# Performance work log

Measured on AMD Instinct MI355X. Metric: run time of the kernel, lower is better.

The kernel has to match this reference:

```python
import jax, jax.numpy as jnp
import numpy as np
from jax import lax

B, N, SEG, T = 64, 19, 15, 400
FIN, HID, K, NH, DM, FF, L, NC = 64, 128, 4, 4, 64, 128, 4, 3
EPS = 1e-5


def setup_inputs() -> dict:
    key = jax.random.key(0)
    ks = jax.random.split(key, 40)
    nrm = lambda i, s, sc=0.05: jax.random.normal(ks[i], s, dtype=jnp.float32) * sc
    inp = {
        "X": jax.random.normal(ks[0], (B, N, SEG, T), dtype=jnp.float32),
        "A_hat": jax.random.uniform(ks[1], (B, K, SEG, N, N), dtype=jnp.float32),
        "conv1_w": nrm(2, (32, 1, 25)), "conv1_b": nrm(3, (32,)),
        "conv2_w": nrm(4, (64, 32, 9)), "conv2_b": nrm(5, (64,)),
        "g1_W": nrm(6, (HID, FIN)), "g1_q": nrm(7, (K,), 1.0),
        "g1_bn_g": jnp.ones((HID,)), "g1_bn_b": jnp.zeros((HID,)),
        "g1_bn_m": jnp.zeros((HID,)), "g1_bn_v": jnp.ones((HID,)),
        "g2_W": nrm(8, (FIN, HID)), "g2_q": nrm(9, (K,), 1.0),
        "g2_bn_g": jnp.ones((FIN,)), "g2_bn_b": jnp.zeros((FIN,)),
        "g2_bn_m": jnp.zeros((FIN,)), "g2_bn_v": jnp.ones((FIN,)),
        "cls_token": nrm(10, (1, 1, DM), 0.02), "pos_emb": nrm(11, (1, SEG + 1, DM), 0.02),
        "t_wqkv": nrm(12, (L, 3 * DM, DM)), "t_bqkv": nrm(13, (L, 3 * DM)),
        "t_wo": nrm(14, (L, DM, DM)), "t_bo": nrm(15, (L, DM)),
        "t_ln1g": jnp.ones((L, DM)), "t_ln1b": jnp.zeros((L, DM)),
        "t_w1": nrm(16, (L, FF, DM)), "t_b1": nrm(17, (L, FF)),
        "t_w2": nrm(18, (L, DM, FF)), "t_b2": nrm(19, (L, DM)),
        "t_ln2g": jnp.ones((L, DM)), "t_ln2b": jnp.zeros((L, DM)),
        "clf_w": nrm(20, (NC, DM)), "clf_b": nrm(21, (NC,)),
    }
    return inp


def _ln(x, g, b):
    mu = x.mean(-1, keepdims=True)
    v = ((x - mu) ** 2).mean(-1, keepdims=True)
    return (x - mu) * lax.rsqrt(v + EPS) * g + b


def _maxpool(x, w):  # x: [M, C, T]
    return lax.reduce_window(x, -jnp.inf, lax.max, (1, 1, w), (1, 1, w), "VALID")


def _temporal_encoder(X, c1w, c1b, c2w, c2b):
    # X: [B, SEG, N, T] -> [B, SEG, N, FIN]
    x = X.reshape(-1, 1, T)
    dn = ("NCH", "OIH", "NCH")
    x = lax.conv_general_dilated(x, c1w, (4,), [(12, 12)], dimension_numbers=dn) + c1b[None, :, None]
    x = _maxpool(jax.nn.relu(x), 4)                      # [M,32,25]
    x = lax.conv_general_dilated(x, c2w, (2,), [(4, 4)], dimension_numbers=dn) + c2b[None, :, None]
    x = _maxpool(jax.nn.relu(x), 2)                      # [M,64,6]
    x = x.mean(-1)                                       # AdaptiveAvgPool1d(1)
    return x.reshape(B, SEG, N, FIN)


def _gcn(Xf, A, W, q, g, b, m, v):
    alpha = jax.nn.softmax(q)                            # [K]
    AX = jnp.einsum("bksnm,bsmf->bksnf", A, Xf)          # K-hop diffusion
    Hk = jnp.einsum("bksnf,of->bksno", AX, W)            # shared linear
    H = jnp.einsum("k,bksno->bsno", alpha, Hk)           # attn-weighted hop mix
    H = (H - m) * lax.rsqrt(v + EPS) * g + b             # eval-mode BatchNorm1d
    return jax.nn.relu(H)


def _forward(X, A_hat, conv1_w, conv1_b, conv2_w, conv2_b,
             g1_W, g1_q, g1_bn_g, g1_bn_b, g1_bn_m, g1_bn_v,
             g2_W, g2_q, g2_bn_g, g2_bn_b, g2_bn_m, g2_bn_v,
             cls_token, pos_emb, t_wqkv, t_bqkv, t_wo, t_bo,
             t_ln1g, t_ln1b, t_w1, t_b1, t_w2, t_b2, t_ln2g, t_ln2b,
             clf_w, clf_b):
    Xs = X.reshape(-1, N, SEG, T).transpose(0, 2, 1, 3)  # [B,SEG,N,T]
    feat = _temporal_encoder(Xs, conv1_w, conv1_b, conv2_w, conv2_b)
    H = _gcn(feat, A_hat, g1_W, g1_q, g1_bn_g, g1_bn_b, g1_bn_m, g1_bn_v)
    H = _gcn(H, A_hat, g2_W, g2_q, g2_bn_g, g2_bn_b, g2_bn_m, g2_bn_v)
    g = H.mean(axis=2)                                   # node-mean -> [B,SEG,DM]
    x = jnp.concatenate([jnp.broadcast_to(cls_token, (B, 1, DM)), g], axis=1)
    x = x + pos_emb[:, : SEG + 1]
    dh = DM // NH
    for l in range(L):
        qkv = x @ t_wqkv[l].T + t_bqkv[l]
        qh, kh, vh = [u.reshape(B, SEG + 1, NH, dh).transpose(0, 2, 1, 3)
                      for u in jnp.split(qkv, 3, axis=-1)]
        attn = jax.nn.softmax(jnp.einsum("bhqd,bhkd->bhqk", qh, kh) / jnp.sqrt(jnp.float32(dh)), axis=-1)
        o = jnp.einsum("bhqk,bhkd->bhqd", attn, vh).transpose(0, 2, 1, 3).reshape(B, SEG + 1, DM)
        x = _ln(x + o @ t_wo[l].T + t_bo[l], t_ln1g[l], t_ln1b[l])
        ff = jax.nn.relu(x @ t_w1[l].T + t_b1[l]) @ t_w2[l].T + t_b2[l]
        x = _ln(x + ff, t_ln2g[l], t_ln2b[l])
    return x[:, 0] @ clf_w.T + clf_b                     # [B, NC]


def reference(X, A_hat, conv1_w, conv1_b, conv2_w, conv2_b,
              g1_W, g1_q, g1_bn_g, g1_bn_b, g1_bn_m, g1_bn_v,
              g2_W, g2_q, g2_bn_g, g2_bn_b, g2_bn_m, g2_bn_v,
              cls_token, pos_emb, t_wqkv, t_bqkv, t_wo, t_bo,
              t_ln1g, t_ln1b, t_w1, t_b1, t_w2, t_b2, t_ln2g, t_ln2b,
              clf_w, clf_b):
    return _forward(X, A_hat, conv1_w, conv1_b, conv2_w, conv2_b,
                    g1_W, g1_q, g1_bn_g, g1_bn_b, g1_bn_m, g1_bn_v,
                    g2_W, g2_q, g2_bn_g, g2_bn_b, g2_bn_m, g2_bn_v,
                    cls_token, pos_emb, t_wqkv, t_bqkv, t_wo, t_bo,
                    t_ln1g, t_ln1b, t_w1, t_b1, t_w2, t_b2, t_ln2g, t_ln2b,
                    clf_w, clf_b)
```

## Files before the change

### kernel.cpp

```cpp
#include <hip/hip_runtime.h>
#include <cmath>

#define B_ 64
#define N_ 19
#define SEG_ 15
#define T_ 400
#define FIN_ 64
#define HID_ 128
#define K_ 4
#define NH_ 4
#define DM_ 64
#define FF_ 128
#define L_ 4
#define NC_ 3
#define EPS_ 1e-5f

typedef __attribute__((ext_vector_type(8))) short bf16x8;
typedef __attribute__((ext_vector_type(4))) short bf16x4;
typedef __attribute__((ext_vector_type(4))) float f32x4;
typedef unsigned short ushort_t;

__device__ __forceinline__ ushort_t f2bf(float x) {
  union { float f; unsigned u; } a; a.f = x;
  unsigned r = a.u + 0x7fffu + ((a.u >> 16) & 1u);
  return (ushort_t)(r >> 16);
}
__device__ __forceinline__ float bf2f(ushort_t h) {
  union { unsigned u; float f; } a; a.u = ((unsigned)h) << 16;
  return a.f;
}

__global__ __launch_bounds__(256) void k_prep(
    const float* __restrict__ c1w, const float* __restrict__ c2w,
    const float* __restrict__ wqkv, const float* __restrict__ wo,
    const float* __restrict__ w1, const float* __restrict__ w2,
    const float* __restrict__ g1W, const float* __restrict__ g2W,
    ushort_t* __restrict__ bt,
    ushort_t* __restrict__ Th, ushort_t* __restrict__ Tl,
    ushort_t* __restrict__ W1h, ushort_t* __restrict__ W1l,
    ushort_t* __restrict__ W2h, ushort_t* __restrict__ W2l,
    ushort_t* __restrict__ C1h, ushort_t* __restrict__ C1l) {
  int gid = blockIdx.x * 256 + threadIdx.x;
  if (gid < 18944) {
    int oc = gid / 296, k = gid - oc * 296;
    int ic = k & 31, kk = k >> 5;
    ushort_t v = 0;
    if (kk < 9) v = f2bf(c2w[oc * 288 + ic * 9 + kk]);
    bt[gid] = v;
  } else if (gid < 68096) {
    int i = gid - 18944;
    int l = i / 12288, r = i % 12288;
    float v = wqkv[i];
    ushort_t h = f2bf(v);
    int dst = l * 32768 + r;
    Th[dst] = h; Tl[dst] = f2bf(v - bf2f(h));
  } else if (gid < 84480) {
    int i = gid - 68096;
    int l = i / 4096, r = i % 4096;
    float v = wo[i];
    ushort_t h = f2bf(v);
    int dst = l * 32768 + 12288 + r;
    Th[dst] = h; Tl[dst] = f2bf(v - bf2f(h));
  } else if (gid < 117248) {
    int i = gid - 84480;
    int l = i / 8192, r = i % 8192;
    float v = w1[i];
    ushort_t h = f2bf(v);
    int dst = l * 32768 + 16384 + r;
    Th[dst] = h; Tl[dst] = f2bf(v - bf2f(h));
  } else if (gid < 150016) {
    int i = gid - 117248;
    int l = i / 8192, r = i % 8192;
    float v = w2[i];
    ushort_t h = f2bf(v);
    int dst = l * 32768 + 24576 + r;
    Th[dst] = h; Tl[dst] = f2bf(v - bf2f(h));
  } else if (gid < 158208) {
    int i = gid - 150016;
    float v = g1W[i];
    ushort_t h = f2bf(v);
    W1h[i] = h;
    W1l[i] = f2bf(v - bf2f(h));
  } else if (gid < 166400) {
    int i = gid - 158208;
    float v = g2W[i];
    ushort_t h = f2bf(v);
    W2h[i] = h;
    W2l[i] = f2bf(v - bf2f(h));
  } else if (gid < 167424) {
    int i = gid - 166400;
    int oc = i >> 5, kk = i & 31;
    float v = (kk < 25) ? c1w[oc * 25 + kk] : 0.f;
    ushort_t h = f2bf(v);
    C1h[i] = h;
    C1l[i] = f2bf(v - bf2f(h));
  }
}

#define RPB 4
#define ICP 40
#define P1R 40
#define OFF_XPH 0
#define OFF_XPL 3840
#define OFF_P1  7680
#define SMEM_T  20480

__global__ __launch_bounds__(256, 4) void k_temporal(
    const float* __restrict__ X, const float* __restrict__ c1b,
    const float* __restrict__ c2b,
    const ushort_t* __restrict__ C1h, const ushort_t* __restrict__ C1l,
    const ushort_t* __restrict__ BmatT, float* __restrict__ Xf) {
  __shared__ __align__(16) unsigned char smem[SMEM_T];
  ushort_t* xph = (ushort_t*)(smem + OFF_XPH);
  ushort_t* xpl = (ushort_t*)(smem + OFF_XPL);
  ushort_t* p1T = (ushort_t*)(smem + OFF_P1);
  float* Dbuf = (float*)smem;

  const int tid = threadIdx.x;
  const int row0 = blockIdx.x * RPB;
  const int lane = tid & 63, wv = tid >> 6;
  const int quad = lane >> 4, nl = lane & 15;

  for (int i = tid; i < 3200; i += 256) ((unsigned*)p1T)[i] = 0u;
  for (int r = 0; r < RPB; ++r) {
    const int gr = row0 + r;
    const int n = gr % N_;
    const int s = (gr / N_) % SEG_;
    const int b = gr / (N_ * SEG_);
    const float* xin = X + (((size_t)b * N_ + n) * SEG_ + s) * T_ - 12;
    for (int i = tid; i < 480; i += 256) {
      float v = (i >= 12 && i < 412) ? xin[i] : 0.f;
      ushort_t h = f2bf(v);
      xph[r * 480 + i] = h;
      xpl[r * 480 + i] = f2bf(v - bf2f(h));
    }
  }
  __syncthreads();

  {
    bf16x8 bh0 = *(const bf16x8*)(C1h + nl * 32 + quad * 8);
    bf16x8 bh1 = *(const bf16x8*)(C1h + (16 + nl) * 32 + quad * 8);
    bf16x8 bl0 = *(const bf16x8*)(C1l + nl * 32 + quad * 8);
    bf16x8 bl1 = *(const bf16x8*)(C1l + (16 + nl) * 32 + quad * 8);
    const float bias0 = c1b[nl], bias1 = c1b[16 + nl];
    for (int t = wv; t < 28; t += 4) {
      const int r = t / 7, mt = t - r * 7;
      const int aoff = r * 480 + mt * 64 + nl * 4 + quad * 8;
      union { bf16x4 q[2]; bf16x8 v; } ah, al;
      ah.q[0] = *(const bf16x4*)(xph + aoff);
      ah.q[1] = *(const bf16x4*)(xph + aoff + 4);
      al.q[0] = *(const bf16x4*)(xpl + aoff);
      al.q[1] = *(const bf16x4*)(xpl + aoff + 4);
      f32x4 a0 = (f32x4){0.f, 0.f, 0.f, 0.f};
      a0 = __builtin_amdgcn_mfma_f32_16x16x32_bf16(ah.v, bh0, a0, 0, 0, 0);
      a0 = __builtin_amdgcn_mfma_f32_16x16x32_bf16(al.v, bh0, a0, 0, 0, 0);
      a0 = __builtin_amdgcn_mfma_f32_16x16x32_bf16(ah.v, bl0, a0, 0, 0, 0);
      f32x4 a1 = (f32x4){0.f, 0.f, 0.f, 0.f};
      a1 = __builtin_amdgcn_mfma_f32_16x16x32_bf16(ah.v, bh1, a1, 0, 0, 0);
      a1 = __builtin_amdgcn_mfma_f32_16x16x32_bf16(al.v, bh1, a1, 0, 0, 0);
      a1 = __builtin_amdgcn_mfma_f32_16x16x32_bf16(ah.v, bl1, a1, 0, 0, 0);
      const int j = mt * 4 + quad;
      if (j < 25) {
        float m0 = fmaxf(fmaxf(a0[0], a0[1]), fmaxf(a0[2], a0[3]));
        float m1 = fmaxf(fmaxf(a1[0], a1[1]), fmaxf(a1[2], a1[3]));
        p1T[(r * P1R + j + 4) * ICP + nl] = f2bf(fmaxf(m0 + bias0, 0.f));
        p1T[(r * P1R + j + 4) * ICP + 16 + nl] = f2bf(fmaxf(m1 + bias1, 0.f));
      }
    }
  }
  __syncthreads();

  f32x4 acc[4];
  int abase[4];
#pragma unroll
  for (int tm = 0; tm < 4; ++tm) {
    acc[tm] = (f32x4){0.f, 0.f, 0.f, 0.f};
    int m = tm * 16 + nl;
    int rl = m / 14;
    int op = m - rl * 14;
    if (rl > 3) rl = 3;
    if (op > 13) op = 13;
    abase[tm] = (rl * P1R + 2 * op) * ICP + quad * 8;
  }
  const ushort_t* brow = BmatT + (wv * 16 + nl) * 296 + quad * 8;
#pragma unroll
  for (int kk = 0; kk < 9; ++kk) {
    bf16x8 bfr = *(const bf16x8*)(brow + kk * 32);
#pragma unroll
    for (int tm = 0; tm < 4; ++tm) {
      bf16x8 afr = *(const bf16x8*)(p1T + abase[tm] + kk * ICP);
      acc[tm] = __builtin_amdgcn_mfma_f32_16x16x32_bf16(afr, bfr, acc[tm], 0, 0, 0);
    }
  }
  __syncthreads();

#pragma unroll
  for (int tm = 0; tm < 4; ++tm)
#pragma unroll
    for (int rg = 0; rg < 4; ++rg)
      Dbuf[(tm * 16 + quad * 4 + rg) * 66 + wv * 16 + nl] = acc[tm][rg];
  __syncthreads();

  for (int o = tid; o < RPB * 64; o += 256) {
    int rl = o >> 6, oc = o & 63;
    float bias = c2b[oc];
    const float* dr = Dbuf + (rl * 14) * 66 + oc;
    float s = 0.f;
#pragma unroll
    for (int jj = 0; jj < 6; ++jj) {
      float v = fmaxf(dr[(2 * jj) * 66], dr[(2 * jj + 1) * 66]) + bias;
      s += fmaxf(v, 0.f);
    }
    Xf[(size_t)(row0 + rl) * FIN_ + oc] = s * (1.f / 6.f);
  }
}

__global__ __launch_bounds__(256, 2) void k_gcn(
    const float* __restrict__ A, const float* __restrict__ Xf,
    const ushort_t* __restrict__ W1h, const ushort_t* __restrict__ W1l,
    const ushort_t* __restrict__ W2h, const ushort_t* __restrict__ W2l,
    const float* __restrict__ q1, const float* __restrict__ q2,
    const float* __restrict__ b1g, const float* __restrict__ b1b,
    const float* __restrict__ b1m, const float* __restrict__ b1v,
    const float* __restrict__ b2g, const float* __restrict__ b2b,
    const float* __restrict__ b2m, const float* __restrict__ b2v,
    float* __restrict__ G) {
  const int bs = blockIdx.x;
  const int b = bs / SEG_;
  const int s = bs % SEG_;
  const int tid = threadIdx.x;
  const int lane = tid & 63, wv = tid >> 6;
  const int quad = lane >> 4, nl = lane & 15;

  __shared__ __align__(16) ushort_t xh[32 * 72], xl[32 * 72];
  __shared__ __align__(16) ushort_t Hh[32 * 136], Hl[32 * 136];
  __shared__ __align__(16) ushort_t a1h[32 * 40], a1l[32 * 40];
  __shared__ __align__(16) ushort_t a2h[32 * 40], a2l[32 * 40];
  __shared__ __align__(16) ushort_t yTh[128 * 40], yTl[128 * 40];
  __shared__ float zbuf[N_ * 64];
  __shared__ float sc1[HID_], sh1[HID_], sc2[FIN_], sh2[FIN_];

  for (int i = tid; i < 32 * 72 / 2; i += 256) {
    ((unsigned*)xh)[i] = 0u; ((unsigned*)xl)[i] = 0u;
  }
  for (int i = tid; i < 32 * 136 / 2; i += 256) {
    ((unsigned*)Hh)[i] = 0u; ((unsigned*)Hl)[i] = 0u;
  }
  for (int i = tid; i < 32 * 40 / 2; i += 256) {
    ((unsigned*)a1h)[i] = 0u; ((unsigned*)a1l)[i] = 0u;
    ((unsigned*)a2h)[i] = 0u; ((unsigned*)a2l)[i] = 0u;
  }
  for (int o = tid; o < HID_; o += 256) {
    float sc = b1g[o] * rsqrtf(b1v[o] + EPS_);
    sc1[o] = sc; sh1[o] = b1b[o] - b1m[o] * sc;
  }
  for (int o = tid; o < FIN_; o += 256) {
    float sc = b2g[o] * rsqrtf(b2v[o] + EPS_);
    sc2[o] = sc; sh2[o] = b2b[o] - b2m[o] * sc;
  }
  __syncthreads();

  {
    float p0 = q1[0], p1 = q1[1], p2 = q1[2], p3 = q1[3];
    float mx = fmaxf(fmaxf(p0, p1), fmaxf(p2, p3));
    float e0 = expf(p0 - mx), e1 = expf(p1 - mx), e2 = expf(p2 - mx), e3 = expf(p3 - mx);
    float inv = 1.f / (e0 + e1 + e2 + e3);
    float a0 = e0 * inv, a1 = e1 * inv, a2 = e2 * inv, a3 = e3 * inv;
    float r0 = q2[0], r1 = q2[1], r2 = q2[2], r3 = q2[3];
    float mx2 = fmaxf(fmaxf(r0, r1), fmaxf(r2, r3));
    float f0 = expf(r0 - mx2), f1 = expf(r1 - mx2), f2 = expf(r2 - mx2), f3 = expf(r3 - mx2);
    float inv2 = 1.f / (f0 + f1 + f2 + f3);
    float c0 = f0 * inv2, c1 = f1 * inv2, c2 = f2 * inv2, c3 = f3 * inv2;
    const size_t kstride = (size_t)SEG_ * N_ * N_;
    const float* Ab = A + ((size_t)b * K_ * SEG_ + s) * (N_ * N_);
    for (int i = tid; i < N_ * N_; i += 256) {
      int n = i / N_, m = i - n * N_;
      float v0 = Ab[i], v1 = Ab[i + kstride], v2 = Ab[i + 2 * kstride], v3 = Ab[i + 3 * kstride];
      float w1v = a0 * v0 + a1 * v1 + a2 * v2 + a3 * v3;
      float w2v = c0 * v0 + c1 * v1 + c2 * v2 + c3 * v3;
      ushort_t h1 = f2bf(w1v);
      a1h[n * 40 + m] = h1; a1l[n * 40 + m] = f2bf(w1v - bf2f(h1));
      ushort_t h2 = f2bf(w2v);
      a2h[n * 40 + m] = h2; a2l[n * 40 + m] = f2bf(w2v - bf2f(h2));
    }
  }
  {
    const float* xb = Xf + (size_t)bs * N_ * FIN_;
    for (int i = tid; i < N_ * FIN_; i += 256) {
      int r = i >> 6, f = i & 63;
      float v = xb[i];
      ushort_t h = f2bf(v);
      xh[r * 72 + f] = h;
      xl[r * 72 + f] = f2bf(v - bf2f(h));
    }
  }
  __syncthreads();

#pragma unroll
  for (int mtl = 0; mtl < 2; ++mtl) {
    const int om = (wv * 2 + mtl) * 16;
#pragma unroll
    for (int nt = 0; nt < 2; ++nt) {
      f32x4 acc = (f32x4){0.f, 0.f, 0.f, 0.f};
#pragma unroll
      for (int ks = 0; ks < 2; ++ks) {
        bf16x8 ah = *(const bf16x8*)(W1h + (om + nl) * 64 + ks * 32 + quad * 8);
        bf16x8 al = *(const bf16x8*)(W1l + (om + nl) * 64 + ks * 32 + quad * 8);
        bf16x8 bh = *(const bf16x8*)(xh + (nt * 16 + nl) * 72 + ks * 32 + quad * 8);
        bf16x8 bl = *(const bf16x8*)(xl + (nt * 16 + nl) * 72 + ks * 32 + quad * 8);
        acc = __builtin_amdgcn_mfma_f32_16x16x32_bf16(ah, bh, acc, 0, 0, 0);
        acc = __builtin_amdgcn_mfma_f32_16x16x32_bf16(al, bh, acc, 0, 0, 0);
        acc = __builtin_amdgcn_mfma_f32_16x16x32_bf16(ah, bl, acc, 0, 0, 0);
      }
#pragma unroll
      for (int r = 0; r < 4; ++r) {
        int o = om + quad * 4 + r, node = nt * 16 + nl;
        float v = acc[r];
        ushort_t hh = f2bf(v);
        yTh[o * 40 + node] = hh;
        yTl[o * 40 + node] = f2bf(v - bf2f(hh));
      }
    }
  }
  __syncthreads();

#pragma unroll
  for (int mt = 0; mt < 2; ++mt) {
#pragma unroll
    for (int ntl = 0; ntl < 2; ++ntl) {
      const int nt = wv * 2 + ntl;
      f32x4 acc = (f32x4){0.f, 0.f, 0.f, 0.f};
      bf16x8 ah = *(const bf16x8*)(a1h + (mt * 16 + nl) * 40 + quad * 8);
      bf16x8 al = *(const bf16x8*)(a1l + (mt * 16 + nl) * 40 + quad * 8);
      bf16x8 bh = *(const bf16x8*)(yTh + (nt * 16 + nl) * 40 + quad * 8);
      bf16x8 bl = *(const bf16x8*)(yTl + (nt * 16 + nl) * 40 + quad * 8);
      acc = __builtin_amdgcn_mfma_f32_16x16x32_bf16(ah, bh, acc, 0, 0, 0);
      acc = __builtin_amdgcn_mfma_f32_16x16x32_bf16(al, bh, acc, 0, 0, 0);
      acc = __builtin_amdgcn_mfma_f32_16x16x32_bf16(ah, bl, acc, 0, 0, 0);
      const int o = nt * 16 + nl;
      const float sc = sc1[o], sh = sh1[o];
#pragma unroll
      for (int r = 0; r < 4; ++r) {
        int node = mt * 16 + quad * 4 + r;
        if (node < N_) {
          float h = fmaxf(acc[r] * sc + sh, 0.f);
          ushort_t hh = f2bf(h);
          Hh[node * 136 + o] = hh;
          Hl[node * 136 + o] = f2bf(h - bf2f(hh));
        }
      }
    }
  }
  __syncthreads();

  {
    const int om = wv * 16;
#pragma unroll
    for (int nt = 0; nt < 2; ++nt) {
      f32x4 acc = (f32x4){0.f, 0.f, 0.f, 0.f};
#pragma unroll
      for (int ks = 0; ks < 4; ++ks) {
        bf16x8 ah = *(const bf16x8*)(W2h + (om + nl) * 128 + ks * 32 + quad * 8);
        bf16x8 al = *(const bf16x8*)(W2l + (om + nl) * 128 + ks * 32 + quad * 8);
        bf16x8 bh = *(const bf16x8*)(Hh + (nt * 16 + nl) * 136 + ks * 32 + quad * 8);
        bf16x8 bl = *(const bf16x8*)(Hl + (nt * 16 + nl) * 136 + ks * 32 + quad * 8);
        acc = __builtin_amdgcn_mfma_f32_16x16x32_bf16(ah, bh, acc, 0, 0, 0);
        acc = __builtin_amdgcn_mfma_f32_16x16x32_bf16(al, bh, acc, 0, 0, 0);
        acc = __builtin_amdgcn_mfma_f32_16x16x32_bf16(ah, bl, acc, 0, 0, 0);
      }
#pragma unroll
      for (int r = 0; r < 4; ++r) {
        int o2 = om + quad * 4 + r, node = nt * 16 + nl;
        float v = acc[r];
        ushort_t hh = f2bf(v);
        yTh[o2 * 40 + node] = hh;
        yTl[o2 * 40 + node] = f2bf(v - bf2f(hh));
      }
    }
  }
  __syncthreads();

#pragma unroll
  for (int mt = 0; mt < 2; ++mt) {
    f32x4 acc = (f32x4){0.f, 0.f, 0.f, 0.f};
    bf16x8 ah = *(const bf16x8*)(a2h + (mt * 16 + nl) * 40 + quad * 8);
    bf16x8 al = *(const bf16x8*)(a2l + (mt * 16 + nl) * 40 + quad * 8);
    bf16x8 bh = *(const bf16x8*)(yTh + (wv * 16 + nl) * 40 + quad * 8);
    bf16x8 bl = *(const bf16x8*)(yTl + (wv * 16 + nl) * 40 + quad * 8);
    acc = __builtin_amdgcn_mfma_f32_16x16x32_bf16(ah, bh, acc, 0, 0, 0);
    acc = __builtin_amdgcn_mfma_f32_16x16x32_bf16(al, bh, acc, 0, 0, 0);
    acc = __builtin_amdgcn_mfma_f32_16x16x32_bf16(ah, bl, acc, 0, 0, 0);
    const int o2 = wv * 16 + nl;
    const float sc = sc2[o2], sh = sh2[o2];
#pragma unroll
    for (int r = 0; r < 4; ++r) {
      int node = mt * 16 + quad * 4 + r;
      if (node < N_)
        zbuf[node * 64 + o2] = fmaxf(acc[r] * sc + sh, 0.f);
    }
  }
  __syncthreads();

  if (tid < FIN_) {
    float ssum = 0.f;
#pragma unroll
    for (int nn = 0; nn < N_; ++nn) ssum += zbuf[nn * 64 + tid];
    G[(size_t)bs * FIN_ + tid] = ssum * (1.f / (float)N_);
  }
}

__global__ __launch_bounds__(64, 1) void k_transformer(
    const float* __restrict__ G, const float* __restrict__ cls,
    const float* __restrict__ pos,
    const ushort_t* __restrict__ Th, const ushort_t* __restrict__ Tl,
    const float* __restrict__ bqkv, const float* __restrict__ bo,
    const float* __restrict__ ln1g, const float* __restrict__ ln1b,
    const float* __restrict__ b1, const float* __restrict__ b2,
    const float* __restrict__ ln2g, const float* __restrict__ ln2b,
    const float* __restrict__ clfw, const float* __restrict__ clfb,
    float* __restrict__ out) {
  const int b = blockIdx.x;
  const int lane = threadIdx.x;
  const int quad = lane >> 4, nl = lane & 15;

  __shared__ float xbuf[16 * 64];
  __shared__ __align__(16) ushort_t xh[16 * 72], xl[16 * 72];
  __shared__ float qkvb[16 * 196];
  __shared__ float scb[16 * 17];
  __shared__ __align__(16) ushort_t oh[16 * 72], ol[16 * 72];
  __shared__ __align__(16) ushort_t h1h[16 * 136], h1l[16 * 136];
  __shared__ float tmpb[16 * 64];

#pragma unroll
  for (int g = 0; g < 4; ++g) {
    const int t = g * 4 + quad;
    float4 base = (t == 0) ? ((const float4*)cls)[nl]
                           : ((const float4*)(G + ((size_t)b * SEG_ + (t - 1)) * DM_))[nl];
    float4 p = ((const float4*)(pos + t * DM_))[nl];
    float4 v;
    v.x = base.x + p.x; v.y = base.y + p.y;
    v.z = base.z + p.z; v.w = base.w + p.w;
    ((float4*)(xbuf + t * 64))[nl] = v;
    const int bi = t * 72 + nl * 4;
    ushort_t h0 = f2bf(v.x), h1 = f2bf(v.y), h2 = f2bf(v.z), h3 = f2bf(v.w);
    xh[bi + 0] = h0; xh[bi + 1] = h1; xh[bi + 2] = h2; xh[bi + 3] = h3;
    xl[bi + 0] = f2bf(v.x - bf2f(h0));
    xl[bi + 1] = f2bf(v.y - bf2f(h1));
    xl[bi + 2] = f2bf(v.z - bf2f(h2));
    xl[bi + 3] = f2bf(v.w - bf2f(h3));
  }

  for (int l = 0; l < L_; ++l) {
    const ushort_t* TH = Th + l * 32768;
    const ushort_t* TL = Tl + l * 32768;

#pragma unroll
    for (int nt = 0; nt < 12; ++nt) {
      f32x4 acc = (f32x4){0.f, 0.f, 0.f, 0.f};
#pragma unroll
      for (int ks = 0; ks < 2; ++ks) {
        bf16x8 ah = *(const bf16x8*)(xh + nl * 72 + ks * 32 + quad * 8);
        bf16x8 al = *(const bf16x8*)(xl + nl * 72 + ks * 32 + quad * 8);
        bf16x8 bh = *(const bf16x8*)(TH + (nt * 16 + nl) * 64 + ks * 32 + quad * 8);
        bf16x8 bl = *(const bf16x8*)(TL + (nt * 16 + nl) * 64 + ks * 32 + quad * 8);
        acc = __builtin_amdgcn_mfma_f32_16x16x32_bf16(ah, bh, acc, 0, 0, 0);
        acc = __builtin_amdgcn_mfma_f32_16x16x32_bf16(al, bh, acc, 0, 0, 0);
        acc = __builtin_amdgcn_mfma_f32_16x16x32_bf16(ah, bl, acc, 0, 0, 0);
      }
      const int j = nt * 16 + nl;
      const float bias = bqkv[l * 192 + j];
#pragma unroll
      for (int r = 0; r < 4; ++r)
        qkvb[(quad * 4 + r) * 196 + j] = acc[r] + bias;
    }

#pragma unroll
    for (int h = 0; h < NH_; ++h) {
      float sc[4];
      const float4* qr = (const float4*)(qkvb + nl * 196 + h * 16);
      float4 q0 = qr[0], q1 = qr[1], q2 = qr[2], q3 = qr[3];
#pragma unroll
      for (int uu = 0; uu < 4; ++uu) {
        const float4* kr = (const float4*)(qkvb + (quad * 4 + uu) * 196 + 64 + h * 16);
        float4 k0 = kr[0], k1 = kr[1], k2 = kr[2], k3 = kr[3];
        float a = q0.x * k0.x + q0.y * k0.y + q0.z * k0.z + q0.w * k0.w
                + q1.x * k1.x + q1.y * k1.y + q1.z * k1.z + q1.w * k1.w
                + q2.x * k2.x + q2.y * k2.y + q2.z * k2.z + q2.w * k2.w
                + q3.x * k3.x + q3.y * k3.y + q3.z * k3.z + q3.w * k3.w;
        sc[uu] = a * 0.25f;
      }
      float mx = fmaxf(fmaxf(sc[0], sc[1]), fmaxf(sc[2], sc[3]));
      mx = fmaxf(mx, __shfl_xor(mx, 16));
      mx = fmaxf(mx, __shfl_xor(mx, 32));
      float e[4];
      float sum = 0.f;
#pragma unroll
      for (int uu = 0; uu < 4; ++uu) { e[uu] = expf(sc[uu] - mx); sum += e[uu]; }
      sum += __shfl_xor(sum, 16);
      sum += __shfl_xor(sum, 32);
      const float is = 1.f / sum;
      float* prow = &scb[nl * 17];
#pragma unroll
      for (int uu = 0; uu < 4; ++uu) prow[quad * 4 + uu] = e[uu] * is;
      float o0 = 0.f, o1 = 0.f, o2 = 0.f, o3 = 0.f;
#pragma unroll
      for (int u = 0; u < 16; ++u) {
        float p = prow[u];
        float4 vv = *(const float4*)(qkvb + u * 196 + 128 + h * 16 + quad * 4);
        o0 += p * vv.x; o1 += p * vv.y; o2 += p * vv.z; o3 += p * vv.w;
      }
      const int eb = nl * 72 + h * 16 + quad * 4;
      ushort_t h0 = f2bf(o0), h1 = f2bf(o1), h2 = f2bf(o2), h3 = f2bf(o3);
      oh[eb + 0] = h0; oh[eb + 1] = h1; oh[eb + 2] = h2; oh[eb + 3] = h3;
      ol[eb + 0] = f2bf(o0 - bf2f(h0));
      ol[eb + 1] = f2bf(o1 - bf2f(h1));
      ol[eb + 2] = f2bf(o2 - bf2f(h2));
      ol[eb + 3] = f2bf(o3 - bf2f(h3));
    }

#pragma unroll
    for (int nt = 0; nt < 4; ++nt) {
      f32x4 acc = (f32x4){0.f, 0.f, 0.f, 0.f};
#pragma unroll
      for (int ks = 0; ks < 2; ++ks) {
        bf16x8 ah = *(const bf16x8*)(oh + nl * 72 + ks * 32 + quad * 8);
        bf16x8 al = *(const bf16x8*)(ol + nl * 72 + ks * 32 + quad * 8);
        bf16x8 bh = *(const bf16x8*)(TH + 12288 + (nt * 16 + nl) * 64 + ks * 32 + quad * 8);
        bf16x8 bl = *(const bf16x8*)(TL + 12288 + (nt * 16 + nl) * 64 + ks * 32 + quad * 8);
        acc = __builtin_amdgcn_mfma_f32_16x16x32_bf16(ah, bh, acc, 0, 0, 0);
        acc = __builtin_amdgcn_mfma_f32_16x16x32_bf16(al, bh, acc, 0, 0, 0);
        acc = __builtin_amdgcn_mfma_f32_16x16x32_bf16(ah, bl, acc, 0, 0, 0);
      }
      const int d = nt * 16 + nl;
      const float bias = bo[l * 64 + d];
#pragma unroll
      for (int r = 0; r < 4; ++r) {
        int t = quad * 4 + r;
        tmpb[t * 64 + d] = xbuf[t * 64 + d] + acc[r] + bias;
      }
    }

#pragma unroll
    for (int g = 0; g < 4; ++g) {
      const int t = g * 4 + quad;
      float4 v = ((const float4*)(tmpb + t * 64))[nl];
      float s = v.x + v.y + v.z + v.w;
      s += __shfl_xor(s, 1); s += __shfl_xor(s, 2);
      s += __shfl_xor(s, 4); s += __shfl_xor(s, 8);
      float mu = s * (1.f / 64.f);
      float d0 = v.x - mu, d1 = v.y - mu, d2 = v.z - mu, d3 = v.w - mu;
      float vr = d0 * d0 + d1 * d1 + d2 * d2 + d3 * d3;
      vr += __shfl_xor(vr, 1); vr += __shfl_xor(vr, 2);
      vr += __shfl_xor(vr, 4); vr += __shfl_xor(vr, 8);
      float rs = rsqrtf(vr * (1.f / 64.f) + EPS_);
      float4 g4 = ((const float4*)(ln1g + l * 64))[nl];
      float4 b4 = ((const float4*)(ln1b + l * 64))[nl];
      float4 o4;
      o4.x = d0 * rs * g4.x + b4.x; o4.y = d1 * rs * g4.y + b4.y;
      o4.z = d2 * rs * g4.z + b4.z; o4.w = d3 * rs * g4.w + b4.w;
      ((float4*)(xbuf + t * 64))[nl] = o4;
      const int bi = t * 72 + nl * 4;
      ushort_t h0 = f2bf(o4.x), h1 = f2bf(o4.y), h2 = f2bf(o4.z), h3 = f2bf(o4.w);
      xh[bi + 0] = h0; xh[bi + 1] = h1; xh[bi + 2] = h2; xh[bi + 3] = h3;
      xl[bi + 0] = f2bf(o4.x - bf2f(h0));
      xl[bi + 1] = f2bf(o4.y - bf2f(h1));
      xl[bi + 2] = f2bf(o4.z - bf2f(h2));
      xl[bi + 3] = f2bf(o4.w - bf2f(h3));
    }

#pragma unroll
    for (int nt = 0; nt < 8; ++nt) {
      f32x4 acc = (f32x4){0.f, 0.f, 0.f, 0.f};
#pragma unroll
      for (int ks = 0; ks < 2; ++ks) {
        bf16x8 ah = *(const bf16x8*)(xh + nl * 72 + ks * 32 + quad * 8);
        bf16x8 al = *(const bf16x8*)(xl + nl * 72 + ks * 32 + quad * 8);
        bf16x8 bh = *(const bf16x8*)(TH + 16384 + (nt * 16 + nl) * 64 + ks * 32 + quad * 8);
        bf16x8 bl = *(const bf16x8*)(TL + 16384 + (nt * 16 + nl) * 64 + ks * 32 + quad * 8);
        acc = __builtin_amdgcn_mfma_f32_16x16x32_bf16(ah, bh, acc, 0, 0, 0);
        acc = __builtin_amdgcn_mfma_f32_16x16x32_bf16(al, bh, acc, 0, 0, 0);
        acc = __builtin_amdgcn_mfma_f32_16x16x32_bf16(ah, bl, acc, 0, 0, 0);
      }
      const int f = nt * 16 + nl;
      const float bias = b1[l * 128 + f];
#pragma unroll
      for (int r = 0; r < 4; ++r) {
        int t = quad * 4 + r;
        float v = fmaxf(acc[r] + bias, 0.f);
        ushort_t hh = f2bf(v);
        h1h[t * 136 + f] = hh;
        h1l[t * 136 + f] = f2bf(v - bf2f(hh));
      }
    }

#pragma unroll
    for (int nt = 0; nt < 4; ++nt) {
      f32x4 acc = (f32x4){0.f, 0.f, 0.f, 0.f};
#pragma unroll
      for (int ks = 0; ks < 4; ++ks) {
        bf16x8 ah = *(const bf16x8*)(h1h + nl * 136 + ks * 32 + quad * 8);
        bf16x8 al = *(const bf16x8*)(h1l + nl * 136 + ks * 32 + quad * 8);
        bf16x8 bh = *(const bf16x8*)(TH + 24576 + (nt * 16 + nl) * 128 + ks * 32 + quad * 8);
        bf16x8 bl = *(const bf16x8*)(TL + 24576 + (nt * 16 + nl) * 128 + ks * 32 + quad * 8);
        acc = __builtin_amdgcn_mfma_f32_16x16x32_bf16(ah, bh, acc, 0, 0, 0);
        acc = __builtin_amdgcn_mfma_f32_16x16x32_bf16(al, bh, acc, 0, 0, 0);
        acc = __builtin_amdgcn_mfma_f32_16x16x32_bf16(ah, bl, acc, 0, 0, 0);
      }
      const int d = nt * 16 + nl;
      const float bias = b2[l * 64 + d];
#pragma unroll
      for (int r = 0; r < 4; ++r) {
        int t = quad * 4 + r;
        tmpb[t * 64 + d] = xbuf[t * 64 + d] + acc[r] + bias;
      }
    }

#pragma unroll
    for (int g = 0; g < 4; ++g) {
      const int t = g * 4 + quad;
      float4 v = ((const float4*)(tmpb + t * 64))[nl];
      float s = v.x + v.y + v.z + v.w;
      s += __shfl_xor(s, 1); s += __shfl_xor(s, 2);
      s += __shfl_xor(s, 4); s += __shfl_xor(s, 8);
      float mu = s * (1.f / 64.f);
      float d0 = v.x - mu, d1 = v.y - mu, d2 = v.z - mu, d3 = v.w - mu;
      float vr = d0 * d0 + d1 * d1 + d2 * d2 + d3 * d3;
      vr += __shfl_xor(vr, 1); vr += __shfl_xor(vr, 2);
      vr += __shfl_xor(vr, 4); vr += __shfl_xor(vr, 8);
      float rs = rsqrtf(vr * (1.f / 64.f) + EPS_);
      float4 g4 = ((const float4*)(ln2g + l * 64))[nl];
      float4 b4 = ((const float4*)(ln2b + l * 64))[nl];
      float4 o4;
      o4.x = d0 * rs * g4.x + b4.x; o4.y = d1 * rs * g4.y + b4.y;
      o4.z = d2 * rs * g4.z + b4.z; o4.w = d3 * rs * g4.w + b4.w;
      ((float4*)(xbuf + t * 64))[nl] = o4;
      const int bi = t * 72 + nl * 4;
      ushort_t h0 = f2bf(o4.x), h1 = f2bf(o4.y), h2 = f2bf(o4.z), h3 = f2bf(o4.w);
      xh[bi + 0] = h0; xh[bi + 1] = h1; xh[bi + 2] = h2; xh[bi + 3] = h3;
      xl[bi + 0] = f2bf(o4.x - bf2f(h0));
      xl[bi + 1] = f2bf(o4.y - bf2f(h1));
      xl[bi + 2] = f2bf(o4.z - bf2f(h2));
      xl[bi + 3] = f2bf(o4.w - bf2f(h3));
    }
  }

  if (lane < NC_) {
    float acc = clfb[lane];
    const float* wr = &clfw[lane * DM_];
    for (int d = 0; d < DM_; ++d) acc += xbuf[d] * wr[d];
    out[b * NC_ + lane] = acc;
  }
}

extern "C" void kernel_launch(void* const* d_in, const int* in_sizes, int n_in,
                              void* d_out, int out_size, void* d_ws, size_t ws_size,
                              hipStream_t stream) {
  (void)in_sizes; (void)n_in; (void)out_size; (void)ws_size;
  const float* X    = (const float*)d_in[0];
  const float* A    = (const float*)d_in[1];
  const float* c1w  = (const float*)d_in[2];
  const float* c1b  = (const float*)d_in[3];
  const float* c2w  = (const float*)d_in[4];
  const float* c2b  = (const float*)d_in[5];
  const float* g1W  = (const float*)d_in[6];
  const float* g1q  = (const float*)d_in[7];
  const float* g1g  = (const float*)d_in[8];
  const float* g1b  = (const float*)d_in[9];
  const float* g1m  = (const float*)d_in[10];
  const float* g1v  = (const float*)d_in[11];
  const float* g2W  = (const float*)d_in[12];
  const float* g2q  = (const float*)d_in[13];
  const float* g2g  = (const float*)d_in[14];
  const float* g2b  = (const float*)d_in[15];
  const float* g2m  = (const float*)d_in[16];
  const float* g2v  = (const float*)d_in[17];
  const float* cls  = (const float*)d_in[18];
  const float* pos  = (const float*)d_in[19];
  const float* wqkv = (const float*)d_in[20];
  const float* bqkv = (const float*)d_in[21];
  const float* wo   = (const float*)d_in[22];
  const float* bo   = (const float*)d_in[23];
  const float* ln1g = (const float*)d_in[24];
  const float* ln1b = (const float*)d_in[25];
  const float* w1   = (const float*)d_in[26];
  const float* b1   = (const float*)d_in[27];
  const float* w2   = (const float*)d_in[28];
  const float* b2   = (const float*)d_in[29];
  const float* ln2g = (const float*)d_in[30];
  const float* ln2b = (const float*)d_in[31];
  const float* clfw = (const float*)d_in[32];
  const float* clfb = (const float*)d_in[33];
  float* out = (float*)d_out;

  char* wsb = (char*)d_ws;
  ushort_t* BmatT = (ushort_t*)(wsb + 0);
  ushort_t* Th  = (ushort_t*)(wsb + 37888);
  ushort_t* Tl  = (ushort_t*)(wsb + 300032);
  ushort_t* W1h = (ushort_t*)(wsb + 562176);
  ushort_t* W1l = (ushort_t*)(wsb + 578560);
  ushort_t* W2h = (ushort_t*)(wsb + 594944);
  ushort_t* W2l = (ushort_t*)(wsb + 611328);
  ushort_t* C1h = (ushort_t*)(wsb + 627712);
  ushort_t* C1l = (ushort_t*)(wsb + 629760);
  float* Xf   = (float*)(wsb + 631808);
  float* G    = (float*)(wsb + 5301248);

  k_prep<<<654, 256, 0, stream>>>(c1w, c2w, wqkv, wo, w1, w2, g1W, g2W,
                                  BmatT, Th, Tl, W1h, W1l, W2h, W2l, C1h, C1l);
  k_temporal<<<B_ * SEG_ * N_ / RPB, 256, 0, stream>>>(
      X, c1b, c2b, C1h, C1l, BmatT, Xf);
  k_gcn<<<B_ * SEG_, 256, 0, stream>>>(A, Xf, W1h, W1l, W2h, W2l,
                                       g1q, g2q, g1g, g1b, g1m, g1v,
                                       g2g, g2b, g2m, g2v, G);
  k_transformer<<<B_, 64, 0, stream>>>(G, cls, pos, Th, Tl,
                                       bqkv, bo, ln1g, ln1b, b1, b2, ln2g, ln2b,
                                       clfw, clfb, out);
}
```

Baseline: 245.6 us.

## Prefetch transformer weight fragments into registers and interleave MFMA chains

In the transformer layer loop, the weight fragments for QKV, output projection and both FFN matmuls are now loaded from global memory ahead of use. QKV weights are double-buffered across pairs of output tiles, and the other weights are loaded early so the loads overlap the attention and layernorm work. The activation fragments are hoisted out of the tile loops, and two independent accumulators are interleaved so consecutive MFMAs do not depend on each other. Biases and layernorm parameters are also loaded early. The cost is much higher register pressure, which could cause spills or lower occupancy.

```diff
diff --git a/kernel.cpp b/kernel.cpp
--- a/kernel.cpp
+++ b/kernel.cpp
@@ -29,6 +29,7 @@
   union { unsigned u; float f; } a; a.u = ((unsigned)h) << 16;
   return a.f;
 }
+#define MFMA(a, b, c) __builtin_amdgcn_mfma_f32_16x16x32_bf16((a), (b), (c), 0, 0, 0)
 
 __global__ __launch_bounds__(256) void k_prep(
     const float* __restrict__ c1w, const float* __restrict__ c2w,
@@ -152,13 +153,13 @@
       al.q[0] = *(const bf16x4*)(xpl + aoff);
       al.q[1] = *(const bf16x4*)(xpl + aoff + 4);
       f32x4 a0 = (f32x4){0.f, 0.f, 0.f, 0.f};
-      a0 = __builtin_amdgcn_mfma_f32_16x16x32_bf16(ah.v, bh0, a0, 0, 0, 0);
-      a0 = __builtin_amdgcn_mfma_f32_16x16x32_bf16(al.v, bh0, a0, 0, 0, 0);
-      a0 = __builtin_amdgcn_mfma_f32_16x16x32_bf16(ah.v, bl0, a0, 0, 0, 0);
+      a0 = MFMA(ah.v, bh0, a0);
+      a0 = MFMA(al.v, bh0, a0);
+      a0 = MFMA(ah.v, bl0, a0);
       f32x4 a1 = (f32x4){0.f, 0.f, 0.f, 0.f};
-      a1 = __builtin_amdgcn_mfma_f32_16x16x32_bf16(ah.v, bh1, a1, 0, 0, 0);
-      a1 = __builtin_amdgcn_mfma_f32_16x16x32_bf16(al.v, bh1, a1, 0, 0, 0);
-      a1 = __builtin_amdgcn_mfma_f32_16x16x32_bf16(ah.v, bl1, a1, 0, 0, 0);
+      a1 = MFMA(ah.v, bh1, a1);
+      a1 = MFMA(al.v, bh1, a1);
+      a1 = MFMA(ah.v, bl1, a1);
       const int j = mt * 4 + quad;
       if (j < 25) {
         float m0 = fmaxf(fmaxf(a0[0], a0[1]), fmaxf(a0[2], a0[3]));
@@ -189,7 +190,7 @@
 #pragma unroll
     for (int tm = 0; tm < 4; ++tm) {
       bf16x8 afr = *(const bf16x8*)(p1T + abase[tm] + kk * ICP);
-      acc[tm] = __builtin_amdgcn_mfma_f32_16x16x32_bf16(afr, bfr, acc[tm], 0, 0, 0);
+      acc[tm] = MFMA(afr, bfr, acc[tm]);
     }
   }
   __syncthreads();
@@ -308,9 +309,9 @@
         bf16x8 al = *(const bf16x8*)(W1l + (om + nl) * 64 + ks * 32 + quad * 8);
         bf16x8 bh = *(const bf16x8*)(xh + (nt * 16 + nl) * 72 + ks * 32 + quad * 8);
         bf16x8 bl = *(const bf16x8*)(xl + (nt * 16 + nl) * 72 + ks * 32 + quad * 8);
-        acc = __builtin_amdgcn_mfma_f32_16x16x32_bf16(ah, bh, acc, 0, 0, 0);
-        acc = __builtin_amdgcn_mfma_f32_16x16x32_bf16(al, bh, acc, 0, 0, 0);
-        acc = __builtin_amdgcn_mfma_f32_16x16x32_bf16(ah, bl, acc, 0, 0, 0);
+        acc = MFMA(ah, bh, acc);
+        acc = MFMA(al, bh, acc);
+        acc = MFMA(ah, bl, acc);
       }
 #pragma unroll
       for (int r = 0; r < 4; ++r) {
@@ -334,9 +335,9 @@
       bf16x8 al = *(const bf16x8*)(a1l + (mt * 16 + nl) * 40 + quad * 8);
       bf16x8 bh = *(const bf16x8*)(yTh + (nt * 16 + nl) * 40 + quad * 8);
       bf16x8 bl = *(const bf16x8*)(yTl + (nt * 16 + nl) * 40 + quad * 8);
-      acc = __builtin_amdgcn_mfma_f32_16x16x32_bf16(ah, bh, acc, 0, 0, 0);
-      acc = __builtin_amdgcn_mfma_f32_16x16x32_bf16(al, bh, acc, 0, 0, 0);
-      acc = __builtin_amdgcn_mfma_f32_16x16x32_bf16(ah, bl, acc, 0, 0, 0);
+      acc = MFMA(ah, bh, acc);
+      acc = MFMA(al, bh, acc);
+      acc = MFMA(ah, bl, acc);
       const int o = nt * 16 + nl;
       const float sc = sc1[o], sh = sh1[o];
 #pragma unroll
@@ -364,9 +365,9 @@
         bf16x8 al = *(const bf16x8*)(W2l + (om + nl) * 128 + ks * 32 + quad * 8);
         bf16x8 bh = *(const bf16x8*)(Hh + (nt * 16 + nl) * 136 + ks * 32 + quad * 8);
         bf16x8 bl = *(const bf16x8*)(Hl + (nt * 16 + nl) * 136 + ks * 32 + quad * 8);
-        acc = __builtin_amdgcn_mfma_f32_16x16x32_bf16(ah, bh, acc, 0, 0, 0);
-        acc = __builtin_amdgcn_mfma_f32_16x16x32_bf16(al, bh, acc, 0, 0, 0);
-        acc = __builtin_amdgcn_mfma_f32_16x16x32_bf16(ah, bl, acc, 0, 0, 0);
+        acc = MFMA(ah, bh, acc);
+        acc = MFMA(al, bh, acc);
+        acc = MFMA(ah, bl, acc);
       }
 #pragma unroll
       for (int r = 0; r < 4; ++r) {
@@ -387,9 +388,9 @@
     bf16x8 al = *(const bf16x8*)(a2l + (mt * 16 + nl) * 40 + quad * 8);
     bf16x8 bh = *(const bf16x8*)(yTh + (wv * 16 + nl) * 40 + quad * 8);
     bf16x8 bl = *(const bf16x8*)(yTl + (wv * 16 + nl) * 40 + quad * 8);
-    acc = __builtin_amdgcn_mfma_f32_16x16x32_bf16(ah, bh, acc, 0, 0, 0);
-    acc = __builtin_amdgcn_mfma_f32_16x16x32_bf16(al, bh, acc, 0, 0, 0);
-    acc = __builtin_amdgcn_mfma_f32_16x16x32_bf16(ah, bl, acc, 0, 0, 0);
+    acc = MFMA(ah, bh, acc);
+    acc = MFMA(al, bh, acc);
+    acc = MFMA(ah, bl, acc);
     const int o2 = wv * 16 + nl;
     const float sc = sc2[o2], sh = sh2[o2];
 #pragma unroll
@@ -454,25 +455,87 @@
     const ushort_t* TH = Th + l * 32768;
     const ushort_t* TL = Tl + l * 32768;
 
-#pragma unroll
-    for (int nt = 0; nt < 12; ++nt) {
-      f32x4 acc = (f32x4){0.f, 0.f, 0.f, 0.f};
+    {
+      float qb[12];
+#pragma unroll
+      for (int nt = 0; nt < 12; ++nt) qb[nt] = bqkv[l * 192 + nt * 16 + nl];
+      bf16x8 xah[2], xal[2];
 #pragma unroll
       for (int ks = 0; ks < 2; ++ks) {
-        bf16x8 ah = *(const bf16x8*)(xh + nl * 72 + ks * 32 + quad * 8);
-        bf16x8 al = *(const bf16x8*)(xl + nl * 72 + ks * 32 + quad * 8);
-        bf16x8 bh = *(const bf16x8*)(TH + (nt * 16 + nl) * 64 + ks * 32 + quad * 8);
-        bf16x8 bl = *(const bf16x8*)(TL + (nt * 16 + nl) * 64 + ks * 32 + quad * 8);
-        acc = __builtin_amdgcn_mfma_f32_16x16x32_bf16(ah, bh, acc, 0, 0, 0);
-        acc = __builtin_amdgcn_mfma_f32_16x16x32_bf16(al, bh, acc, 0, 0, 0);
-        acc = __builtin_amdgcn_mfma_f32_16x16x32_bf16(ah, bl, acc, 0, 0, 0);
-      }
-      const int j = nt * 16 + nl;
-      const float bias = bqkv[l * 192 + j];
-#pragma unroll
-      for (int r = 0; r < 4; ++r)
-        qkvb[(quad * 4 + r) * 196 + j] = acc[r] + bias;
-    }
+        xah[ks] = *(const bf16x8*)(xh + nl * 72 + ks * 32 + quad * 8);
+        xal[ks] = *(const bf16x8*)(xl + nl * 72 + ks * 32 + quad * 8);
+      }
+      bf16x8 wh[2][2][2], wl[2][2][2];
+#pragma unroll
+      for (int tp = 0; tp < 2; ++tp)
+#pragma unroll
+        for (int ks = 0; ks < 2; ++ks) {
+          wh[0][tp][ks] = *(const bf16x8*)(TH + (tp * 16 + nl) * 64 + ks * 32 + quad * 8);
+          wl[0][tp][ks] = *(const bf16x8*)(TL + (tp * 16 + nl) * 64 + ks * 32 + quad * 8);
+        }
+#pragma unroll
+      for (int pr = 0; pr < 6; ++pr) {
+        const int cb = pr & 1, nb = cb ^ 1;
+        if (pr < 5) {
+#pragma unroll
+          for (int tp = 0; tp < 2; ++tp)
+#pragma unroll
+            for (int ks = 0; ks < 2; ++ks) {
+              const int nt = (pr + 1) * 2 + tp;
+              wh[nb][tp][ks] = *(const bf16x8*)(TH + (nt * 16 + nl) * 64 + ks * 32 + quad * 8);
+              wl[nb][tp][ks] = *(const bf16x8*)(TL + (nt * 16 + nl) * 64 + ks * 32 + quad * 8);
+            }
+        }
+        f32x4 a0 = (f32x4){0.f, 0.f, 0.f, 0.f};
+        f32x4 a1 = (f32x4){0.f, 0.f, 0.f, 0.f};
+#pragma unroll
+        for (int ks = 0; ks < 2; ++ks) {
+          a0 = MFMA(xah[ks], wh[cb][0][ks], a0);
+          a1 = MFMA(xah[ks], wh[cb][1][ks], a1);
+          a0 = MFMA(xal[ks], wh[cb][0][ks], a0);
+          a1 = MFMA(xal[ks], wh[cb][1][ks], a1);
+          a0 = MFMA(xah[ks], wl[cb][0][ks], a0);
+          a1 = MFMA(xah[ks], wl[cb][1][ks], a1);
+        }
+        const int j0 = (pr * 2) * 16 + nl, j1 = (pr * 2 + 1) * 16 + nl;
+#pragma unroll
+        for (int r = 0; r < 4; ++r) {
+          qkvb[(quad * 4 + r) * 196 + j0] = a0[r] + qb[pr * 2];
+          qkvb[(quad * 4 + r) * 196 + j1] = a1[r] + qb[pr * 2 + 1];
+        }
+      }
+    }
+
+    bf16x8 pwh[2][2][2], pwl[2][2][2];
+#pragma unroll
+    for (int pp = 0; pp < 2; ++pp)
+#pragma unroll
+      for (int tp = 0; tp < 2; ++tp)
+#pragma unroll
+        for (int ks = 0; ks < 2; ++ks) {
+          const int nt = pp * 2 + tp;
+          pwh[pp][tp][ks] = *(const bf16x8*)(TH + 12288 + (nt * 16 + nl) * 64 + ks * 32 + quad * 8);
+          pwl[pp][tp][ks] = *(const bf16x8*)(TL + 12288 + (nt * 16 + nl) * 64 + ks * 32 + quad * 8);
+        }
+    float pb[4];
+#pragma unroll
+    for (int nt = 0; nt < 4; ++nt) pb[nt] = bo[l * 64 + nt * 16 + nl];
+    float4 g1v4 = ((const float4*)(ln1g + l * 64))[nl];
+    float4 b1v4 = ((const float4*)(ln1b + l * 64))[nl];
+    bf16x8 fwh[4][2][2], fwl[4][2][2];
+#pragma unroll
+    for (int pp = 0; pp < 4; ++pp)
+#pragma unroll
+      for (int tp = 0; tp < 2; ++tp)
+#pragma unroll
+        for (int ks = 0; ks < 2; ++ks) {
+          const int nt = pp * 2 + tp;
+          fwh[pp][tp][ks] = *(const bf16x8*)(TH + 16384 + (nt * 16 + nl) * 64 + ks * 32 + quad * 8);
+          fwl[pp][tp][ks] = *(const bf16x8*)(TL + 16384 + (nt * 16 + nl) * 64 + ks * 32 + quad * 8);
+        }
+    float fb[8];
+#pragma unroll
+    for (int nt = 0; nt < 8; ++nt) fb[nt] = b1[l * 128 + nt * 16 + nl];
 
 #pragma unroll
     for (int h = 0; h < NH_; ++h) {
@@ -518,27 +581,52 @@
       ol[eb + 3] = f2bf(o3 - bf2f(h3));
     }
 
-#pragma unroll
-    for (int nt = 0; nt < 4; ++nt) {
-      f32x4 acc = (f32x4){0.f, 0.f, 0.f, 0.f};
+    {
+      bf16x8 oah[2], oal[2];
 #pragma unroll
       for (int ks = 0; ks < 2; ++ks) {
-        bf16x8 ah = *(const bf16x8*)(oh + nl * 72 + ks * 32 + quad * 8);
-        bf16x8 al = *(const bf16x8*)(ol + nl * 72 + ks * 32 + quad * 8);
-        bf16x8 bh = *(const bf16x8*)(TH + 12288 + (nt * 16 + nl) * 64 + ks * 32 + quad * 8);
-        bf16x8 bl = *(const bf16x8*)(TL + 12288 + (nt * 16 + nl) * 64 + ks * 32 + quad * 8);
-        acc = __builtin_amdgcn_mfma_f32_16x16x32_bf16(ah, bh, acc, 0, 0, 0);
-        acc = __builtin_amdgcn_mfma_f32_16x16x32_bf16(al, bh, acc, 0, 0, 0);
-        acc = __builtin_amdgcn_mfma_f32_16x16x32_bf16(ah, bl, acc, 0, 0, 0);
-      }
-      const int d = nt * 16 + nl;
-      const float bias = bo[l * 64 + d];
-#pragma unroll
-      for (int r = 0; r < 4; ++r) {
-        int t = quad * 4 + r;
-        tmpb[t * 64 + d] = xbuf[t * 64 + d] + acc[r] + bias;
-      }
-    }
+        oah[ks] = *(const bf16x8*)(oh + nl * 72 + ks * 32 + quad * 8);
+        oal[ks] = *(const bf16x8*)(ol + nl * 72 + ks * 32 + quad * 8);
+      }
+#pragma unroll
+      for (int pp = 0; pp < 2; ++pp) {
+        f32x4 a0 = (f32x4){0.f, 0.f, 0.f, 0.f};
+        f32x4 a1 = (f32x4){0.f, 0.f, 0.f, 0.f};
+#pragma unroll
+        for (int ks = 0; ks < 2; ++ks) {
+          a0 = MFMA(oah[ks], pwh[pp][0][ks], a0);
+          a1 = MFMA(oah[ks], pwh[pp][1][ks], a1);
+          a0 = MFMA(oal[ks], pwh[pp][0][ks], a0);
+          a1 = MFMA(oal[ks], pwh[pp][1][ks], a1);
+          a0 = MFMA(oah[ks], pwl[pp][0][ks], a0);
+          a1 = MFMA(oah[ks], pwl[pp][1][ks], a1);
+        }
+        const int d0 = (pp * 2) * 16 + nl, d1 = (pp * 2 + 1) * 16 + nl;
+#pragma unroll
+        for (int r = 0; r < 4; ++r) {
+          int t = quad * 4 + r;
+          tmpb[t * 64 + d0] = xbuf[t * 64 + d0] + a0[r] + pb[pp * 2];
+          tmpb[t * 64 + d1] = xbuf[t * 64 + d1] + a1[r] + pb[pp * 2 + 1];
+        }
+      }
+    }
+
+    bf16x8 gwh[2][2][4], gwl[2][2][4];
+#pragma unroll
+    for (int pp = 0; pp < 2; ++pp)
+#pragma unroll
+      for (int tp = 0; tp < 2; ++tp)
+#pragma unroll
+        for (int ks = 0; ks < 4; ++ks) {
+          const int nt = pp * 2 + tp;
+          gwh[pp][tp][ks] = *(const bf16x8*)(TH + 24576 + (nt * 16 + nl) * 128 + ks * 32 + quad * 8);
+          gwl[pp][tp][ks] = *(const bf16x8*)(TL + 24576 + (nt * 16 + nl) * 128 + ks * 32 + quad * 8);
+        }
+    float gb[4];
+#pragma unroll
+    for (int nt = 0; nt < 4; ++nt) gb[nt] = b2[l * 64 + nt * 16 + nl];
+    float4 g2v4 = ((const float4*)(ln2g + l * 64))[nl];
+    float4 b2v4 = ((const float4*)(ln2b + l * 64))[nl];
 
 #pragma unroll
     for (int g = 0; g < 4; ++g) {
@@ -553,11 +641,9 @@
       vr += __shfl_xor(vr, 1); vr += __shfl_xor(vr, 2);
       vr += __shfl_xor(vr, 4); vr += __shfl_xor(vr, 8);
       float rs = rsqrtf(vr * (1.f / 64.f) + EPS_);
-      float4 g4 = ((const float4*)(ln1g + l * 64))[nl];
-      float4 b4 = ((const float4*)(ln1b + l * 64))[nl];
       float4 o4;
-      o4.x = d0 * rs * g4.x + b4.x; o4.y = d1 * rs * g4.y + b4.y;
-      o4.z = d2 * rs * g4.z + b4.z; o4.w = d3 * rs * g4.w + b4.w;
+      o4.x = d0 * rs * g1v4.x + b1v4.x; o4.y = d1 * rs * g1v4.y + b1v4.y;
+      o4.z = d2 * rs * g1v4.z + b1v4.z; o4.w = d3 * rs * g1v4.w + b1v4.w;
       ((float4*)(xbuf + t * 64))[nl] = o4;
       const int bi = t * 72 + nl * 4;
       ushort_t h0 = f2bf(o4.x), h1 = f2bf(o4.y), h2 = f2bf(o4.z), h3 = f2bf(o4.w);
@@ -568,50 +654,68 @@
       xl[bi + 3] = f2bf(o4.w - bf2f(h3));
     }
 
-#pragma unroll
-    for (int nt = 0; nt < 8; ++nt) {
-      f32x4 acc = (f32x4){0.f, 0.f, 0.f, 0.f};
+    {
+      bf16x8 xah[2], xal[2];
 #pragma unroll
       for (int ks = 0; ks < 2; ++ks) {
-        bf16x8 ah = *(const bf16x8*)(xh + nl * 72 + ks * 32 + quad * 8);
-        bf16x8 al = *(const bf16x8*)(xl + nl * 72 + ks * 32 + quad * 8);
-        bf16x8 bh = *(const bf16x8*)(TH + 16384 + (nt * 16 + nl) * 64 + ks * 32 + quad * 8);
-        bf16x8 bl = *(const bf16x8*)(TL + 16384 + (nt * 16 + nl) * 64 + ks * 32 + quad * 8);
-        acc = __builtin_amdgcn_mfma_f32_16x16x32_bf16(ah, bh, acc, 0, 0, 0);
-        acc = __builtin_amdgcn_mfma_f32_16x16x32_bf16(al, bh, acc, 0, 0, 0);
-        acc = __builtin_amdgcn_mfma_f32_16x16x32_bf16(ah, bl, acc, 0, 0, 0);
-      }
-      const int f = nt * 16 + nl;
-      const float bias = b1[l * 128 + f];
-#pragma unroll
-      for (int r = 0; r < 4; ++r) {
-        int t = quad * 4 + r;
-        float v = fmaxf(acc[r] + bias, 0.f);
-        ushort_t hh = f2bf(v);
-        h1h[t * 136 + f] = hh;
-        h1l[t * 136 + f] = f2bf(v - bf2f(hh));
-      }
-    }
-
-#pragma unroll
-    for (int nt = 0; nt < 4; ++nt) {
-      f32x4 acc = (f32x4){0.f, 0.f, 0.f, 0.f};
+        xah[ks] = *(const bf16x8*)(xh + nl * 72 + ks * 32 + quad * 8);
+        xal[ks] = *(const bf16x8*)(xl + nl * 72 + ks * 32 + quad * 8);
+      }
+#pragma unroll
+      for (int pp = 0; pp < 4; ++pp) {
+        f32x4 a0 = (f32x4){0.f, 0.f, 0.f, 0.f};
+        f32x4 a1 = (f32x4){0.f, 0.f, 0.f, 0.f};
+#pragma unroll
+        for (int ks = 0; ks < 2; ++ks) {
+          a0 = MFMA(xah[ks], fwh[pp][0][ks], a0);
+          a1 = MFMA(xah[ks], fwh[pp][1][ks], a1);
+          a0 = MFMA(xal[ks], fwh[pp][0][ks], a0);
+          a1 = MFMA(xal[ks], fwh[pp][1][ks], a1);
+          a0 = MFMA(xah[ks], fwl[pp][0][ks], a0);
+          a1 = MFMA(xah[ks], fwl[pp][1][ks], a1);
+        }
+        const int f0 = (pp * 2) * 16 + nl, f1 = (pp * 2 + 1) * 16 + nl;
+#pragma unroll
+        for (int r = 0; r < 4; ++r) {
+          int t = quad * 4 + r;
+          float v0 = fmaxf(a0[r] + fb[pp * 2], 0.f);
+          float v1 = fmaxf(a1[r] + fb[pp * 2 + 1], 0.f);
+          ushort_t hh0 = f2bf(v0), hh1 = f2bf(v1);
+          h1h[t * 136 + f0] = hh0;
+          h1l[t * 136 + f0] = f2bf(v0 - bf2f(hh0));
+          h1h[t * 136 + f1] = hh1;
+          h1l[t * 136 + f1] = f2bf(v1 - bf2f(hh1));
+        }
+      }
+    }
+
+    {
+      bf16x8 hah[4], hal[4];
 #pragma unroll
       for (int ks = 0; ks < 4; ++ks) {
-        bf16x8 ah = *(const bf16x8*)(h1h + nl * 136 + ks * 32 + quad * 8);
-        bf16x8 al = *(const bf16x8*)(h1l + nl * 136 + ks * 32 + quad * 8);
-        bf16x8 bh = *(const bf16x8*)(TH + 24576 + (nt * 16 + nl) * 128 + ks * 32 + quad * 8);
-        bf16x8 bl = *(const bf16x8*)(TL + 24576 + (nt * 16 + nl) * 128 + ks * 32 + quad * 8);
-        acc = __builtin_amdgcn_mfma_f32_16x16x32_bf16(ah, bh, acc, 0, 0, 0);
-        acc = __builtin_amdgcn_mfma_f32_16x16x32_bf16(al, bh, acc, 0, 0, 0);
-        acc = __builtin_amdgcn_mfma_f32_16x16x32_bf16(ah, bl, acc, 0, 0, 0);
-      }
-      const int d = nt * 16 + nl;
-      const float bias = b2[l * 64 + d];
-#pragma unroll
-      for (int r = 0; r < 4; ++r) {
-        int t = quad * 4 + r;
-        tmpb[t * 64 + d] = xbuf[t * 64 + d] + acc[r] + bias;
+        hah[ks] = *(const bf16x8*)(h1h + nl * 136 + ks * 32 + quad * 8);
+        hal[ks] = *(const bf16x8*)(h1l + nl * 136 + ks * 32 + quad * 8);
+      }
+#pragma unroll
+      for (int pp = 0; pp < 2; ++pp) {
+        f32x4 a0 = (f32x4){0.f, 0.f, 0.f, 0.f};
+        f32x4 a1 = (f32x4){0.f, 0.f, 0.f, 0.f};
+#pragma unroll
+        for (int ks = 0; ks < 4; ++ks) {
+          a0 = MFMA(hah[ks], gwh[pp][0][ks], a0);
+          a1 = MFMA(hah[ks], gwh[pp][1][ks], a1);
+          a0 = MFMA(hal[ks], gwh[pp][0][ks], a0);
+          a1 = MFMA(hal[ks], gwh[pp][1][ks], a1);
+          a0 = MFMA(hah[ks], gwl[pp][0][ks], a0);
+          a1 = MFMA(hah[ks], gwl[pp][1][ks], a1);
+        }
+        const int d0 = (pp * 2) * 16 + nl, d1 = (pp * 2 + 1) * 16 + nl;
+#pragma unroll
+        for (int r = 0; r < 4; ++r) {
+          int t = quad * 4 + r;
+          tmpb[t * 64 + d0] = xbuf[t * 64 + d0] + a0[r] + gb[pp * 2];
+          tmpb[t * 64 + d1] = xbuf[t * 64 + d1] + a1[r] + gb[pp * 2 + 1];
+        }
       }
     }
 
@@ -628,11 +732,9 @@
       vr += __shfl_xor(vr, 1); vr += __shfl_xor(vr, 2);
       vr += __shfl_xor(vr, 4); vr += __shfl_xor(vr, 8);
       float rs = rsqrtf(vr * (1.f / 64.f) + EPS_);
-      float4 g4 = ((const float4*)(ln2g + l * 64))[nl];
-      float4 b4 = ((const float4*)(ln2b + l * 64))[nl];
       float4 o4;
-      o4.x = d0 * rs * g4.x + b4.x; o4.y = d1 * rs * g4.y + b4.y;
-      o4.z = d2 * rs * g4.z + b4.z; o4.w = d3 * rs * g4.w + b4.w;
+      o4.x = d0 * rs * g2v4.x + b2v4.x; o4.y = d1 * rs * g2v4.y + b2v4.y;
+      o4.z = d2 * rs * g2v4.z + b2v4.z; o4.w = d3 * rs * g2v4.w + b2v4.w;
       ((float4*)(xbuf + t * 64))[nl] = o4;
       const int bi = t * 72 + nl * 4;
       ushort_t h0 = f2bf(o4.x), h1 = f2bf(o4.y), h2 = f2bf(o4.z), h3 = f2bf(o4.w);
```

Result: slower. 251.4 us (+2.3%).
